# Kernel tuning notes

Measured on AMD Instinct MI355X. Metric: run time of the kernel, lower is better.

## Reference

```python
import jax, jax.numpy as jnp
import numpy as np

BS = 512          # graphs in batch
G = 5             # n_freq_bands
EL = 32           # electrodes per graph
IN = 5            # in_channels
HC = 64           # first_hc == hidden_channels
N = BS * G * EL   # 81920 nodes
E = N * 16        # 1310720 edges
NC = 3            # n_classes
NUM_LAYERS = 2


def setup_inputs() -> dict:
    key = jax.random.key(0)
    ks = jax.random.split(key, 16)
    s = 0.05
    return {
        "x": jax.random.normal(ks[0], (N, IN), jnp.float32),
        "edge_index": jax.random.randint(ks[1], (2, E), 0, N, dtype=jnp.int32),
        "edge_attr": jax.random.uniform(ks[2], (E,), jnp.float32),
        # GatedGraphConv propagation weights: [num_layers, HC, HC]
        "Wg": jax.random.normal(ks[3], (NUM_LAYERS, HC, HC), jnp.float32) * s,
        # GRUCell params (torch layout: gates r,z,n stacked)
        "w_ih": jax.random.normal(ks[4], (3 * HC, HC), jnp.float32) * s,
        "w_hh": jax.random.normal(ks[5], (3 * HC, HC), jnp.float32) * s,
        "b_ih": jnp.zeros((3 * HC,), jnp.float32),
        "b_hh": jnp.zeros((3 * HC,), jnp.float32),
        # MLP head (torch Linear layout: [out, in])
        "W1": jax.random.normal(ks[6], (HC, G * EL * HC), jnp.float32) * s,
        "b1": jnp.zeros((HC,), jnp.float32),
        "W2": jax.random.normal(ks[7], (HC // 2, HC), jnp.float32) * s,
        "b2": jnp.zeros((HC // 2,), jnp.float32),
        "W3": jax.random.normal(ks[8], (HC // 4, HC // 2), jnp.float32) * s,
        "b3": jnp.zeros((HC // 4,), jnp.float32),
        "W4": jax.random.normal(ks[9], (NC, HC // 4), jnp.float32) * s,
        "b4": jnp.zeros((NC,), jnp.float32),
    }


def _gru_cell(m, h, w_ih, w_hh, b_ih, b_hh):
    gi = m @ w_ih.T + b_ih
    gh = h @ w_hh.T + b_hh
    i_r, i_z, i_n = jnp.split(gi, 3, axis=-1)
    h_r, h_z, h_n = jnp.split(gh, 3, axis=-1)
    r = jax.nn.sigmoid(i_r + h_r)
    z = jax.nn.sigmoid(i_z + h_z)
    n = jnp.tanh(i_n + r * h_n)
    return (1.0 - z) * n + z * h


def reference(x, edge_index, edge_attr, Wg, w_ih, w_hh, b_ih, b_hh,
              W1, b1, W2, b2, W3, b3, W4, b4):
    # GatedGraphConv: zero-pad input features to HC
    h = jnp.pad(x, ((0, 0), (0, HC - IN)))  # [N, HC]
    src, dst = edge_index[0], edge_index[1]
    for i in range(NUM_LAYERS):
        m = h @ Wg[i]                               # [N, HC]
        msg = m[src] * edge_attr[:, None]           # [E, HC] gather + weight
        aggr = jax.ops.segment_sum(msg, dst, num_segments=N)  # scatter-add
        h = _gru_cell(aggr, h, w_ih, w_hh, b_ih, b_hh)
    # rearrange '(bs g e) f -> bs (e g f)'
    h = h.reshape(BS, G, EL, HC).transpose(0, 2, 1, 3).reshape(BS, EL * G * HC)
    z = jax.nn.relu(h @ W1.T + b1)
    z = jax.nn.relu(z @ W2.T + b2)
    z = jax.nn.relu(z @ W3.T + b3)
    logits = z @ W4.T + b4
    return jax.nn.softmax(logits, axis=-1)
```

## Files before the change

### kernel.cpp

```cpp
#include <hip/hip_runtime.h>
#include <cstdint>

#define BSZ 512
#define NG 5
#define NEL 32
#define IN_C 5
#define HC 64
#define NN (BSZ * NG * NEL)
#define NE (NN * 16)
#define NC 3
#define KTOT (NG * NEL * HC)
#define NSLICE 16
#define NCB 320
#define CCHUNK (NE / NCB)
#define SORTCAP 5120

typedef __attribute__((ext_vector_type(8))) short bf16x8;
typedef __attribute__((ext_vector_type(4))) float f32x4;

__device__ __forceinline__ float bcast(float v, int l) {
  return __int_as_float(__builtin_amdgcn_readlane(__float_as_int(v), l));
}

__device__ __forceinline__ ushort bf16r(float f) {
  unsigned u = __float_as_uint(f);
  return (ushort)((u + 0x7FFFu + ((u >> 16) & 1u)) >> 16);
}

__device__ __forceinline__ float bf16f(ushort s) {
  return __uint_as_float(((unsigned)s) << 16);
}

__device__ __forceinline__ float sigmoidf_(float x) {
  return 1.0f / (1.0f + __expf(-x));
}

__device__ __forceinline__ float tanhf_(float x) {
  x = fminf(fmaxf(x, -15.0f), 15.0f);
  float e = __expf(2.0f * x);
  return (e - 1.0f) / (e + 1.0f);
}

__global__ void k_init(const float* __restrict__ x, ushort* __restrict__ hb) {
  int idx = blockIdx.x * 256 + threadIdx.x;
  int n = idx >> 6, c = idx & 63;
  hb[idx] = (c < IN_C) ? bf16r(x[n * IN_C + c]) : (ushort)0;
}

__global__ void k_cvtw(const float* __restrict__ W1, ushort* __restrict__ w1b) {
  int i = blockIdx.x * 256 + threadIdx.x;
  w1b[i] = bf16r(W1[i]);
}

__global__ void __launch_bounds__(256) k_chist(const int* __restrict__ ei,
                                               int* __restrict__ ghist) {
  __shared__ int lh[NCB];
  const int t = threadIdx.x;
  for (int i = t; i < NCB; i += 256) lh[i] = 0;
  __syncthreads();
  const int base = blockIdx.x * CCHUNK;
  for (int k = t; k < CCHUNK; k += 256)
    atomicAdd(&lh[ei[NE + base + k] >> 8], 1);
  __syncthreads();
  for (int i = t; i < NCB; i += 256) ghist[i * NCB + blockIdx.x] = lh[i];
}

__global__ void k_cscan(const int* __restrict__ ghist, int* __restrict__ cstart,
                        int* __restrict__ gof) {
  __shared__ int tot[NCB];
  __shared__ int cs[NCB + 1];
  const int t = threadIdx.x;
  if (t < NCB) {
    int s = 0;
    const int* g = ghist + t * NCB;
    for (int blk = 0; blk < NCB; ++blk) s += g[blk];
    tot[t] = s;
  }
  __syncthreads();
  if (t == 0) {
    int run = 0;
    for (int i = 0; i < NCB; ++i) { cs[i] = run; run += tot[i]; }
    cs[NCB] = run;
  }
  __syncthreads();
  if (t < NCB + 1) cstart[t] = cs[t];
  if (t < NCB) {
    int run = cs[t];
    const int* g = ghist + t * NCB;
    int* go = gof + t * NCB;
    for (int blk = 0; blk < NCB; ++blk) { go[blk] = run; run += g[blk]; }
  }
}

__global__ void __launch_bounds__(256) k_cpart(const int* __restrict__ ei,
                                               const float* __restrict__ ea,
                                               const int* __restrict__ gof,
                                               int* __restrict__ ent4,
                                               uchar1* __restrict__ dstlo) {
  __shared__ int cur[NCB];
  const int t = threadIdx.x;
  for (int i = t; i < NCB; i += 256) cur[i] = gof[i * NCB + blockIdx.x];
  __syncthreads();
  const int base = blockIdx.x * CCHUNK;
  for (int k = t; k < CCHUNK; k += 256) {
    int e = base + k;
    int src = ei[e];
    int dst = ei[NE + e];
    ushort bw = bf16r(ea[e]);
    int slot = atomicAdd(&cur[dst >> 8], 1);
    ent4[slot] = src | ((int)bw << 17);
    dstlo[slot].x = (unsigned char)(dst & 255);
  }
}

__global__ void __launch_bounds__(256) k_sort(const int* __restrict__ ent4,
                                              const uchar1* __restrict__ dstlo,
                                              const int* __restrict__ cstart,
                                              int* __restrict__ csr4,
                                              int* __restrict__ off,
                                              int* __restrict__ cnt) {
  __shared__ int nh[256];
  __shared__ int part[256];
  __shared__ int sent[SORTCAP];
  const int t = threadIdx.x;
  const int b = blockIdx.x;
  const int r0 = cstart[b];
  const int r1 = cstart[b + 1];
  int len = r1 - r0;
  if (len > SORTCAP) len = SORTCAP;
  nh[t] = 0;
  __syncthreads();
  for (int k = t; k < len; k += 256) atomicAdd(&nh[dstlo[r0 + k].x], 1);
  __syncthreads();
  int a0 = nh[t];
  part[t] = a0;
  __syncthreads();
  for (int d = 1; d < 256; d <<= 1) {
    int x = (t >= d) ? part[t - d] : 0;
    __syncthreads();
    part[t] += x;
    __syncthreads();
  }
  const int base = part[t] - a0;
  const int n0 = b * 256;
  off[n0 + t] = r0 + base;
  cnt[n0 + t] = a0;
  nh[t] = base;
  __syncthreads();
  for (int k = t; k < len; k += 256) {
    int d = dstlo[r0 + k].x;
    int slot = atomicAdd(&nh[d], 1);
    sent[slot] = ent4[r0 + k];
  }
  __syncthreads();
  for (int k = t; k < len; k += 256) csr4[r0 + k] = sent[k];
}


__global__ void __launch_bounds__(256) k_gemm_mfma(
    const ushort* __restrict__ hb, const float* __restrict__ Wg,
    ushort* __restrict__ m16) {
  const int lane = threadIdx.x & 63;
  const int cl = lane & 15;
  const int quad = lane >> 4;
  bf16x8 B[4][2];
#pragma unroll
  for (int ct = 0; ct < 4; ++ct)
#pragma unroll
    for (int kh = 0; kh < 2; ++kh) {
      bf16x8 b;
#pragma unroll
      for (int j = 0; j < 8; ++j)
        b[j] = (short)bf16r(Wg[(kh * 32 + quad * 8 + j) * 64 + ct * 16 + cl]);
      B[ct][kh] = b;
    }
  int g = (blockIdx.x * 256 + threadIdx.x) >> 6;
  const int nwaves = (gridDim.x * 256) >> 6;
  for (; g < NN / 16; g += nwaves) {
    const ushort* hp = hb + (size_t)(g * 16 + cl) * 64 + quad * 8;
    bf16x8 a0 = *(const bf16x8*)hp;
    bf16x8 a1 = *(const bf16x8*)(hp + 32);
    ushort* mp = m16 + (size_t)(g * 16 + quad * 4) * 64 + cl;
#pragma unroll
    for (int ct = 0; ct < 4; ++ct) {
      f32x4 acc = {0.0f, 0.0f, 0.0f, 0.0f};
      acc = __builtin_amdgcn_mfma_f32_16x16x32_bf16(a0, B[ct][0], acc, 0, 0, 0);
      acc = __builtin_amdgcn_mfma_f32_16x16x32_bf16(a1, B[ct][1], acc, 0, 0, 0);
#pragma unroll
      for (int rg = 0; rg < 4; ++rg)
        mp[(size_t)rg * 64 + ct * 16] = bf16r(acc[rg]);
    }
  }
}

__global__ void k_aggregate(const int* __restrict__ off, const int* __restrict__ cnt,
                            const int* __restrict__ csr4, const ushort* __restrict__ m16,
                            ushort* __restrict__ aggr16) {
  const int lane = threadIdx.x & 63;
  int wv = (blockIdx.x * 256 + threadIdx.x) >> 6;
  const int nw = (gridDim.x * 256) >> 6;
  for (int n = wv; n < NN; n += nw) {
    const int r0 = __builtin_amdgcn_readfirstlane(off[n]);
    const int c = __builtin_amdgcn_readfirstlane(cnt[n]);
    int ed = 0;
    if (lane < c) ed = csr4[r0 + lane];
    const int cc = c > 64 ? 64 : c;
    float acc = 0.0f;
    int i = 0;
    for (; i + 8 <= cc; i += 8) {
      int x0 = __builtin_amdgcn_readlane(ed, i + 0);
      int x1 = __builtin_amdgcn_readlane(ed, i + 1);
      int x2 = __builtin_amdgcn_readlane(ed, i + 2);
      int x3 = __builtin_amdgcn_readlane(ed, i + 3);
      int x4 = __builtin_amdgcn_readlane(ed, i + 4);
      int x5 = __builtin_amdgcn_readlane(ed, i + 5);
      int x6 = __builtin_amdgcn_readlane(ed, i + 6);
      int x7 = __builtin_amdgcn_readlane(ed, i + 7);
      float m0 = bf16f(m16[(size_t)(x0 & 0x1FFFF) * 64 + lane]);
      float m1 = bf16f(m16[(size_t)(x1 & 0x1FFFF) * 64 + lane]);
      float m2 = bf16f(m16[(size_t)(x2 & 0x1FFFF) * 64 + lane]);
      float m3 = bf16f(m16[(size_t)(x3 & 0x1FFFF) * 64 + lane]);
      float m4 = bf16f(m16[(size_t)(x4 & 0x1FFFF) * 64 + lane]);
      float m5 = bf16f(m16[(size_t)(x5 & 0x1FFFF) * 64 + lane]);
      float m6 = bf16f(m16[(size_t)(x6 & 0x1FFFF) * 64 + lane]);
      float m7 = bf16f(m16[(size_t)(x7 & 0x1FFFF) * 64 + lane]);
      acc = fmaf(m0, bf16f((ushort)((unsigned)x0 >> 17)), acc);
      acc = fmaf(m1, bf16f((ushort)((unsigned)x1 >> 17)), acc);
      acc = fmaf(m2, bf16f((ushort)((unsigned)x2 >> 17)), acc);
      acc = fmaf(m3, bf16f((ushort)((unsigned)x3 >> 17)), acc);
      acc = fmaf(m4, bf16f((ushort)((unsigned)x4 >> 17)), acc);
      acc = fmaf(m5, bf16f((ushort)((unsigned)x5 >> 17)), acc);
      acc = fmaf(m6, bf16f((ushort)((unsigned)x6 >> 17)), acc);
      acc = fmaf(m7, bf16f((ushort)((unsigned)x7 >> 17)), acc);
    }
    for (; i < cc; ++i) {
      int x = __builtin_amdgcn_readlane(ed, i);
      acc = fmaf(bf16f(m16[(size_t)(x & 0x1FFFF) * 64 + lane]),
                 bf16f((ushort)((unsigned)x >> 17)), acc);
    }
    for (int j = 64; j < c; ++j) {
      int x = csr4[r0 + j];
      acc = fmaf(bf16f(m16[(size_t)(x & 0x1FFFF) * 64 + lane]),
                 bf16f((ushort)((unsigned)x >> 17)), acc);
    }
    aggr16[(size_t)n * 64 + lane] = bf16r(acc);
  }
}

__global__ void __launch_bounds__(256) k_gru_mfma(
    const ushort* __restrict__ aggr16, ushort* __restrict__ hb,
    const float* __restrict__ wih, const float* __restrict__ whh,
    const float* __restrict__ bih, const float* __restrict__ bhh) {
  const int lane = threadIdx.x & 63;
  const int w = threadIdx.x >> 6;
  const int cl = lane & 15;
  const int quad = lane >> 4;
  const int c = w * 16 + cl;

  bf16x8 BI[3][2], BH[3][2];
#pragma unroll
  for (int g3 = 0; g3 < 3; ++g3) {
    const float* wi = wih + (size_t)(g3 * 64 + c) * 64;
    const float* wh = whh + (size_t)(g3 * 64 + c) * 64;
#pragma unroll
    for (int kh = 0; kh < 2; ++kh) {
      bf16x8 bi, bh;
#pragma unroll
      for (int j = 0; j < 8; ++j) {
        bi[j] = (short)bf16r(wi[kh * 32 + quad * 8 + j]);
        bh[j] = (short)bf16r(wh[kh * 32 + quad * 8 + j]);
      }
      BI[g3][kh] = bi;
      BH[g3][kh] = bh;
    }
  }
  const float br = bih[c] + bhh[c];
  const float bz = bih[64 + c] + bhh[64 + c];
  const float bni = bih[128 + c];
  const float bnh = bhh[128 + c];

  const int ngroups = NN / 16;
  for (int g = blockIdx.x; g < ngroups; g += gridDim.x) {
    const size_t arow = (size_t)(g * 16 + cl) * 64 + quad * 8;
    bf16x8 a0 = *(const bf16x8*)(aggr16 + arow);
    bf16x8 a1 = *(const bf16x8*)(aggr16 + arow + 32);
    bf16x8 h0 = *(const bf16x8*)(hb + arow);
    bf16x8 h1 = *(const bf16x8*)(hb + arow + 32);
    float hv[4];
    const size_t obase = (size_t)(g * 16 + quad * 4) * 64 + c;
#pragma unroll
    for (int rg = 0; rg < 4; ++rg) hv[rg] = bf16f(hb[obase + (size_t)rg * 64]);
    __syncthreads();

    f32x4 zero = {0.0f, 0.0f, 0.0f, 0.0f};
    f32x4 aR = zero, aZ = zero, aN = zero, hR = zero, hZ = zero, hN = zero;
    aR = __builtin_amdgcn_mfma_f32_16x16x32_bf16(a0, BI[0][0], aR, 0, 0, 0);
    aR = __builtin_amdgcn_mfma_f32_16x16x32_bf16(a1, BI[0][1], aR, 0, 0, 0);
    aZ = __builtin_amdgcn_mfma_f32_16x16x32_bf16(a0, BI[1][0], aZ, 0, 0, 0);
    aZ = __builtin_amdgcn_mfma_f32_16x16x32_bf16(a1, BI[1][1], aZ, 0, 0, 0);
    aN = __builtin_amdgcn_mfma_f32_16x16x32_bf16(a0, BI[2][0], aN, 0, 0, 0);
    aN = __builtin_amdgcn_mfma_f32_16x16x32_bf16(a1, BI[2][1], aN, 0, 0, 0);
    hR = __builtin_amdgcn_mfma_f32_16x16x32_bf16(h0, BH[0][0], hR, 0, 0, 0);
    hR = __builtin_amdgcn_mfma_f32_16x16x32_bf16(h1, BH[0][1], hR, 0, 0, 0);
    hZ = __builtin_amdgcn_mfma_f32_16x16x32_bf16(h0, BH[1][0], hZ, 0, 0, 0);
    hZ = __builtin_amdgcn_mfma_f32_16x16x32_bf16(h1, BH[1][1], hZ, 0, 0, 0);
    hN = __builtin_amdgcn_mfma_f32_16x16x32_bf16(h0, BH[2][0], hN, 0, 0, 0);
    hN = __builtin_amdgcn_mfma_f32_16x16x32_bf16(h1, BH[2][1], hN, 0, 0, 0);

#pragma unroll
    for (int rg = 0; rg < 4; ++rg) {
      float r = sigmoidf_(aR[rg] + hR[rg] + br);
      float z = sigmoidf_(aZ[rg] + hZ[rg] + bz);
      float nv = tanhf_(aN[rg] + bni + r * (hN[rg] + bnh));
      hb[obase + (size_t)rg * 64] = bf16r((1.0f - z) * nv + z * hv[rg]);
    }
  }
}

__global__ void __launch_bounds__(256) k_mlp1_mfma(
    const ushort* __restrict__ hb, const ushort* __restrict__ w1b,
    float* __restrict__ part) {
  const int lane = threadIdx.x & 63;
  const int w = threadIdx.x >> 6;
  const int cl = lane & 15;
  const int quad = lane >> 4;
  const int bg = blockIdx.x >> 4;
  const int sl = blockIdx.x & 15;
  const int bs0 = bg * 16;
  const int c = w * 16 + cl;
  f32x4 acc = {0.0f, 0.0f, 0.0f, 0.0f};
#pragma unroll
  for (int e2 = 0; e2 < 2; ++e2) {
    const int e = sl * 2 + e2;
#pragma unroll
    for (int g = 0; g < 5; ++g) {
      const ushort* hp = hb + ((size_t)(bs0 + cl) * 160 + g * 32 + e) * 64 + quad * 8;
      bf16x8 a0 = *(const bf16x8*)hp;
      bf16x8 a1 = *(const bf16x8*)(hp + 32);
      const int kbase = e * 320 + g * 64;
      const ushort* wp = w1b + (size_t)c * KTOT + kbase + quad * 8;
      bf16x8 b0 = *(const bf16x8*)wp;
      bf16x8 b1 = *(const bf16x8*)(wp + 32);
      acc = __builtin_amdgcn_mfma_f32_16x16x32_bf16(a0, b0, acc, 0, 0, 0);
      acc = __builtin_amdgcn_mfma_f32_16x16x32_bf16(a1, b1, acc, 0, 0, 0);
    }
  }
  float* pp = part + ((size_t)sl * BSZ + bs0 + quad * 4) * 64 + c;
#pragma unroll
  for (int rg = 0; rg < 4; ++rg) pp[(size_t)rg * 64] = acc[rg];
}

__global__ void k_tail(const float* __restrict__ part, const float* __restrict__ b1,
                       const float* __restrict__ W2, const float* __restrict__ b2,
                       const float* __restrict__ W3, const float* __restrict__ b3,
                       const float* __restrict__ W4, const float* __restrict__ b4,
                       float* __restrict__ out) {
  const int lane = threadIdx.x & 63;
  const int bs = blockIdx.x * 4 + (threadIdx.x >> 6);
  float zp = 0.0f;
#pragma unroll
  for (int s = 0; s < NSLICE; ++s) zp += part[((size_t)s * BSZ + bs) * 64 + lane];
  float zv = fmaxf(zp + b1[lane], 0.0f);
  const int c2 = lane & 31;
  float acc2 = b2[c2];
#pragma unroll
  for (int k = 0; k < 64; ++k) acc2 = fmaf(bcast(zv, k), W2[c2 * 64 + k], acc2);
  acc2 = fmaxf(acc2, 0.0f);
  const int c3 = lane & 15;
  float acc3 = b3[c3];
#pragma unroll
  for (int k = 0; k < 32; ++k) acc3 = fmaf(bcast(acc2, k), W3[c3 * 32 + k], acc3);
  acc3 = fmaxf(acc3, 0.0f);
  float l0 = b4[0], l1 = b4[1], l2 = b4[2];
#pragma unroll
  for (int k = 0; k < 16; ++k) {
    float v = bcast(acc3, k);
    l0 = fmaf(v, W4[k], l0);
    l1 = fmaf(v, W4[16 + k], l1);
    l2 = fmaf(v, W4[32 + k], l2);
  }
  float mx = fmaxf(l0, fmaxf(l1, l2));
  float e0 = __expf(l0 - mx), e1 = __expf(l1 - mx), e2 = __expf(l2 - mx);
  float inv = 1.0f / (e0 + e1 + e2);
  if (lane == 0) {
    out[bs * 3 + 0] = e0 * inv;
    out[bs * 3 + 1] = e1 * inv;
    out[bs * 3 + 2] = e2 * inv;
  }
}

extern "C" void kernel_launch(void* const* d_in, const int* in_sizes, int n_in,
                              void* d_out, int out_size, void* d_ws, size_t ws_size,
                              hipStream_t stream) {
  const float* x = (const float*)d_in[0];
  const int* ei = (const int*)d_in[1];
  const float* ea = (const float*)d_in[2];
  const float* Wg = (const float*)d_in[3];
  const float* wih = (const float*)d_in[4];
  const float* whh = (const float*)d_in[5];
  const float* bih = (const float*)d_in[6];
  const float* bhh = (const float*)d_in[7];
  const float* W1 = (const float*)d_in[8];
  const float* b1 = (const float*)d_in[9];
  const float* W2 = (const float*)d_in[10];
  const float* b2 = (const float*)d_in[11];
  const float* W3 = (const float*)d_in[12];
  const float* b3 = (const float*)d_in[13];
  const float* W4 = (const float*)d_in[14];
  const float* b4 = (const float*)d_in[15];
  float* out = (float*)d_out;

  float* part = (float*)d_ws;
  int* ghist = (int*)(part + (size_t)NSLICE * BSZ * 64);
  int* gof = ghist + NCB * NCB;
  int* cstart = gof + NCB * NCB;
  int* off = cstart + 324;
  int* cnt = off + NN;
  int* ent4 = cnt + NN;
  int* csr4 = ent4 + NE;
  ushort* hb = (ushort*)(csr4 + NE);
  ushort* m16 = hb + (size_t)NN * 64;
  ushort* aggr16 = m16 + (size_t)NN * 64;
  ushort* w1b = aggr16 + (size_t)NN * 64;
  uchar1* dstlo = (uchar1*)(w1b + (size_t)KTOT * HC);

  k_chist<<<NCB, 256, 0, stream>>>(ei, ghist);
  k_cscan<<<1, 320, 0, stream>>>(ghist, cstart, gof);
  k_cpart<<<NCB, 256, 0, stream>>>(ei, ea, gof, ent4, dstlo);
  k_sort<<<NCB, 256, 0, stream>>>(ent4, dstlo, cstart, csr4, off, cnt);
  k_cvtw<<<KTOT * HC / 256, 256, 0, stream>>>(W1, w1b);

  k_init<<<NN * 64 / 256, 256, 0, stream>>>(x, hb);
  for (int layer = 0; layer < 2; ++layer) {
    k_gemm_mfma<<<1280, 256, 0, stream>>>(hb, Wg + layer * 64 * 64, m16);
    k_aggregate<<<2048, 256, 0, stream>>>(off, cnt, csr4, m16, aggr16);
    k_gru_mfma<<<1280, 256, 0, stream>>>(aggr16, hb, wih, whh, bih, bhh);
  }
  k_mlp1_mfma<<<512, 256, 0, stream>>>(hb, w1b, part);
  k_tail<<<BSZ / 4, 256, 0, stream>>>(part, b1, W2, b2, W3, b3, W4, b4, out);
}
```

Measured before the change: 374.7 us.

## Parallelize bucket-offset scan across blocks and prefetch next node's edges in aggregate

The single-block serial scan over the 320x320 histogram is replaced with a per-row parallel Hillis-Steele scan across 320 blocks, followed by a small scan of the row totals. Partition cursors become the row-local offset plus the bucket start. The aggregate kernel also software-prefetches the next node's offset, count and edge entries while the current node is processed, to hide gather latency. This adds one extra kernel launch and more registers in the aggregate kernel.

Result: faster. 333.4 us (-11.0%).

```diff
diff --git a/kernel.cpp b/kernel.cpp
--- a/kernel.cpp
+++ b/kernel.cpp
@@ -65,41 +65,52 @@
   for (int i = t; i < NCB; i += 256) ghist[i * NCB + blockIdx.x] = lh[i];
 }
 
-__global__ void k_cscan(const int* __restrict__ ghist, int* __restrict__ cstart,
-                        int* __restrict__ gof) {
-  __shared__ int tot[NCB];
-  __shared__ int cs[NCB + 1];
+__global__ void __launch_bounds__(NCB) k_rowscan(const int* __restrict__ ghist,
+                                                 int* __restrict__ gof,
+                                                 int* __restrict__ tot) {
+  __shared__ int part[NCB];
   const int t = threadIdx.x;
-  if (t < NCB) {
-    int s = 0;
-    const int* g = ghist + t * NCB;
-    for (int blk = 0; blk < NCB; ++blk) s += g[blk];
-    tot[t] = s;
-  }
-  __syncthreads();
-  if (t == 0) {
-    int run = 0;
-    for (int i = 0; i < NCB; ++i) { cs[i] = run; run += tot[i]; }
-    cs[NCB] = run;
-  }
-  __syncthreads();
-  if (t < NCB + 1) cstart[t] = cs[t];
-  if (t < NCB) {
-    int run = cs[t];
-    const int* g = ghist + t * NCB;
-    int* go = gof + t * NCB;
-    for (int blk = 0; blk < NCB; ++blk) { go[blk] = run; run += g[blk]; }
-  }
+  const int b = blockIdx.x;
+  const int v = ghist[b * NCB + t];
+  part[t] = v;
+  __syncthreads();
+  for (int d = 1; d < NCB; d <<= 1) {
+    int x = (t >= d) ? part[t - d] : 0;
+    __syncthreads();
+    part[t] += x;
+    __syncthreads();
+  }
+  gof[b * NCB + t] = part[t] - v;
+  if (t == NCB - 1) tot[b] = part[t];
+}
+
+__global__ void __launch_bounds__(NCB) k_cscan2(const int* __restrict__ tot,
+                                                int* __restrict__ cstart) {
+  __shared__ int part[NCB];
+  const int t = threadIdx.x;
+  const int v = tot[t];
+  part[t] = v;
+  __syncthreads();
+  for (int d = 1; d < NCB; d <<= 1) {
+    int x = (t >= d) ? part[t - d] : 0;
+    __syncthreads();
+    part[t] += x;
+    __syncthreads();
+  }
+  cstart[t] = part[t] - v;
+  if (t == NCB - 1) cstart[NCB] = part[t];
 }
 
 __global__ void __launch_bounds__(256) k_cpart(const int* __restrict__ ei,
                                                const float* __restrict__ ea,
                                                const int* __restrict__ gof,
+                                               const int* __restrict__ cstart,
                                                int* __restrict__ ent4,
                                                uchar1* __restrict__ dstlo) {
   __shared__ int cur[NCB];
   const int t = threadIdx.x;
-  for (int i = t; i < NCB; i += 256) cur[i] = gof[i * NCB + blockIdx.x];
+  for (int i = t; i < NCB; i += 256)
+    cur[i] = gof[i * NCB + blockIdx.x] + cstart[i];
   __syncthreads();
   const int base = blockIdx.x * CCHUNK;
   for (int k = t; k < CCHUNK; k += 256) {
@@ -199,11 +210,21 @@
   const int lane = threadIdx.x & 63;
   int wv = (blockIdx.x * 256 + threadIdx.x) >> 6;
   const int nw = (gridDim.x * 256) >> 6;
+  int r0c = 0, cC = 0, edc = 0;
+  if (wv < NN) {
+    r0c = __builtin_amdgcn_readfirstlane(off[wv]);
+    cC = __builtin_amdgcn_readfirstlane(cnt[wv]);
+    if (lane < cC) edc = csr4[r0c + lane];
+  }
   for (int n = wv; n < NN; n += nw) {
-    const int r0 = __builtin_amdgcn_readfirstlane(off[n]);
-    const int c = __builtin_amdgcn_readfirstlane(cnt[n]);
-    int ed = 0;
-    if (lane < c) ed = csr4[r0 + lane];
+    const int r0 = r0c, c = cC, ed = edc;
+    const int n2 = n + nw;
+    if (n2 < NN) {
+      r0c = __builtin_amdgcn_readfirstlane(off[n2]);
+      cC = __builtin_amdgcn_readfirstlane(cnt[n2]);
+      edc = 0;
+      if (lane < cC) edc = csr4[r0c + lane];
+    }
     const int cc = c > 64 ? 64 : c;
     float acc = 0.0f;
     int i = 0;
@@ -413,7 +434,8 @@
   float* part = (float*)d_ws;
   int* ghist = (int*)(part + (size_t)NSLICE * BSZ * 64);
   int* gof = ghist + NCB * NCB;
-  int* cstart = gof + NCB * NCB;
+  int* tot = gof + NCB * NCB;
+  int* cstart = tot + NCB;
   int* off = cstart + 324;
   int* cnt = off + NN;
   int* ent4 = cnt + NN;
@@ -425,8 +447,9 @@
   uchar1* dstlo = (uchar1*)(w1b + (size_t)KTOT * HC);
 
   k_chist<<<NCB, 256, 0, stream>>>(ei, ghist);
-  k_cscan<<<1, 320, 0, stream>>>(ghist, cstart, gof);
-  k_cpart<<<NCB, 256, 0, stream>>>(ei, ea, gof, ent4, dstlo);
+  k_rowscan<<<NCB, NCB, 0, stream>>>(ghist, gof, tot);
+  k_cscan2<<<1, NCB, 0, stream>>>(tot, cstart);
+  k_cpart<<<NCB, 256, 0, stream>>>(ei, ea, gof, cstart, ent4, dstlo);
   k_sort<<<NCB, 256, 0, stream>>>(ent4, dstlo, cstart, csr4, off, cnt);
   k_cvtw<<<KTOT * HC / 256, 256, 0, stream>>>(W1, w1b);
 
```
